# Kernel tuning notes

Measured on AMD Instinct MI355X. Metric: run time of the kernel, lower is better.

Reference implementation:

```python
import jax, jax.numpy as jnp
import numpy as np

N = 100000   # nodes
E = 1600000  # random edges per augmented graph (before self-loops)
F = 128      # input_dim
H = 128      # hidden_dim
K = 3        # n_clusters
L = 3        # num_layers


def setup_inputs() -> dict:
    key = jax.random.key(0)
    ks = jax.random.split(key, 24)
    x1 = jax.random.normal(ks[0], (N, F), jnp.float32)
    x2 = jax.random.normal(ks[1], (N, F), jnp.float32)
    x3 = jax.random.normal(ks[2], (N, F), jnp.float32)
    loops = jnp.arange(N, dtype=jnp.int32)
    self_loops = jnp.stack([loops, loops])  # [2, N]

    def aug_edges(k):
        e = jax.random.randint(k, (2, E), 0, N, dtype=jnp.int32)
        return jnp.concatenate([e, self_loops], axis=1)  # [2, E+N]

    e1 = aug_edges(ks[3])
    e2 = aug_edges(ks[4])
    e3 = aug_edges(ks[5])

    s = 1.0 / np.sqrt(H)
    Ws = jax.random.normal(ks[6], (L, H, H), jnp.float32) * s  # F == H
    bs = jnp.zeros((L, H), jnp.float32)
    a = jnp.float32(0.25)  # PReLU slope (torch default)
    cw1 = jax.random.normal(ks[7], (H, H), jnp.float32) * s
    cb1 = jnp.zeros((H,), jnp.float32)
    cw2 = jax.random.normal(ks[8], (H, K), jnp.float32) * s
    cb2 = jnp.zeros((K,), jnp.float32)
    iw1 = jax.random.normal(ks[9], (H, H), jnp.float32) * s
    ib1 = jnp.zeros((H,), jnp.float32)
    iw2 = jax.random.normal(ks[10], (H, H), jnp.float32) * s
    ib2 = jnp.zeros((H,), jnp.float32)
    return dict(x1=x1, x2=x2, x3=x3, e1=e1, e2=e2, e3=e3,
                Ws=Ws, bs=bs, a=a, cw1=cw1, cb1=cb1, cw2=cw2, cb2=cb2,
                iw1=iw1, ib1=ib1, iw2=iw2, ib2=ib2)


def _l2norm(z):
    # F.normalize(z, dim=1), eps=1e-12
    return z / jnp.maximum(jnp.linalg.norm(z, axis=1, keepdims=True), 1e-12)


def _gconv(x, edges, Ws, bs, a):
    # DGL GraphConv norm='left': messages from src scaled by 1/out_deg(src),
    # summed at dst, then linear + shared PReLU per layer; final row L2-norm.
    src, dst = edges[0], edges[1]
    deg = jax.ops.segment_sum(jnp.ones(src.shape[0], x.dtype), src, num_segments=N)
    inv = 1.0 / jnp.maximum(deg, 1.0)  # DGL clamps zero out-degree
    z = x
    for l in range(L):
        msg = (z * inv[:, None])[src]               # [E, H] gather
        agg = jax.ops.segment_sum(msg, dst, num_segments=N)  # [N, H] scatter-add
        z = agg @ Ws[l] + bs[l]
        z = jnp.where(z >= 0, z, a * z)             # PReLU
    return _l2norm(z)


def reference(x1, x2, x3, e1, e2, e3, Ws, bs, a,
              cw1, cb1, cw2, cb2, iw1, ib1, iw2, ib2):
    z1 = _gconv(x1, e1, Ws, bs, a)
    z2 = _gconv(x2, e2, Ws, bs, a)
    z3 = _gconv(x3, e3, Ws, bs, a)

    def cluster(z):
        h = jax.nn.elu(z @ cw1 + cb1)
        p = jax.nn.softmax(h @ cw2 + cb2, axis=1)
        return _l2norm(p)

    def inst(z):
        return jax.nn.elu(z @ iw1 + ib1) @ iw2 + ib2

    return (z3, inst(z1), inst(z2), cluster(z1), cluster(z2))
```

## Files before the change

### kernel.cpp

```cpp
#include <hip/hip_runtime.h>
#include <hip/hip_bf16.h>
#include <cmath>


typedef __attribute__((ext_vector_type(8))) short short8;
typedef __attribute__((ext_vector_type(4))) float floatx4;

#define NB_MAX 512
#define PART_B 256
#define LCSR_MAX 6144

static __device__ __forceinline__ unsigned short f2bf(float f) {
  unsigned u = __builtin_bit_cast(unsigned, f);
  u += 0x7fffu + ((u >> 16) & 1u);
  return (unsigned short)(u >> 16);
}
static __device__ __forceinline__ float bf2f(unsigned short h) {
  unsigned u = ((unsigned)h) << 16;
  return __builtin_bit_cast(float, u);
}
static __device__ __forceinline__ float bflo(unsigned v) {
  return __builtin_bit_cast(float, v << 16);
}
static __device__ __forceinline__ float bfhi(unsigned v) {
  return __builtin_bit_cast(float, v & 0xffff0000u);
}

static __device__ __forceinline__ floatx4 mfma16(short8 a, short8 b, floatx4 c) {
  return __builtin_amdgcn_mfma_f32_16x16x32_bf16(a, b, c, 0, 0, 0);
}


__global__ __launch_bounds__(256) void bucket_count(const int* __restrict__ src,
                                                    const int* __restrict__ dst,
                                                    int ne, int nb, int chunk,
                                                    int* __restrict__ bcnt,
                                                    int* __restrict__ deg) {
  __shared__ int h[NB_MAX];
  const int t = threadIdx.x, b = blockIdx.x;
  for (int i = t; i < nb; i += 256) h[i] = 0;
  __syncthreads();
  const int start = b * chunk, endi = min(start + chunk, ne);
  for (int i = start + t; i < endi; i += 256) {
    atomicAdd(&h[dst[i] >> 8], 1);
    atomicAdd(&deg[src[i]], 1);
  }
  __syncthreads();
  for (int i = t; i < nb; i += 256) bcnt[i * PART_B + b] = h[i];
}

__global__ __launch_bounds__(256) void partition_edges(
    const int* __restrict__ src, const int* __restrict__ dst, int ne, int nb,
    int chunk, const int* __restrict__ boff, int* __restrict__ part) {
  __shared__ int h[NB_MAX];
  const int t = threadIdx.x, b = blockIdx.x;
  for (int i = t; i < nb; i += 256) h[i] = boff[i * PART_B + b];
  __syncthreads();
  const int start = b * chunk, endi = min(start + chunk, ne);
  for (int i = start + t; i < endi; i += 256) {
    int d = dst[i];
    int gpos = atomicAdd(&h[d >> 8], 1);
    part[gpos] = (src[i] << 8) | (d & 255);
  }
}

__global__ __launch_bounds__(256) void fine_csr(const int* __restrict__ part,
                                                const int* __restrict__ boff,
                                                int nb, int n, int ne,
                                                int* __restrict__ row_ptr,
                                                int* __restrict__ csr) {
  __shared__ int s[256];
  __shared__ int cur[256];
  __shared__ int lcsr[LCSR_MAX];
  const int t = threadIdx.x, b2 = blockIdx.x;
  const int base = boff[b2 * PART_B];
  const int endb = boff[(b2 + 1) * PART_B];
  const int cnt_local = endb - base;
  const int node_base = b2 << 8;

  s[t] = 0;
  __syncthreads();
  for (int i = base + t; i < endb; i += 256) atomicAdd(&s[part[i] & 255], 1);
  __syncthreads();
  for (int d = 1; d < 256; d <<= 1) {
    int v = s[t];
    int a = (t >= d) ? s[t - d] : 0;
    __syncthreads();
    s[t] = v + a;
    __syncthreads();
  }
  int excl = (t == 0) ? 0 : s[t - 1];
  int node = node_base + t;
  if (node <= n) row_ptr[node] = base + excl;
  if (b2 == nb - 1 && t == 0) row_ptr[n] = ne;
  cur[t] = excl;
  __syncthreads();

  if (cnt_local <= LCSR_MAX) {
    for (int i = base + t; i < endb; i += 256) {
      int v = part[i];
      int p = atomicAdd(&cur[v & 255], 1);
      lcsr[p] = v >> 8;
    }
    __syncthreads();
    for (int i = t; i < cnt_local; i += 256) csr[base + i] = lcsr[i];
  } else {
    for (int i = base + t; i < endb; i += 256) {
      int v = part[i];
      int p = atomicAdd(&cur[v & 255], 1);
      csr[base + p] = v >> 8;
    }
  }
}

__global__ __launch_bounds__(256) void make_inv(const int* __restrict__ deg,
                                                float* __restrict__ inv, int n) {
  int i = blockIdx.x * blockDim.x + threadIdx.x;
  if (i < n) inv[i] = 1.0f / (float)(deg[i] + 1);
}

#define SCAN_B 256
#define SCAN_T 256

__global__ __launch_bounds__(SCAN_T) void scan_part(const int* __restrict__ cnt,
                                                    int n, int cpt,
                                                    int* __restrict__ partials) {
  __shared__ int red[SCAN_T];
  const int t = threadIdx.x, b = blockIdx.x;
  const int g = b * SCAN_T + t;
  const int start = g * cpt, endi = min(start + cpt, n);
  int s = 0;
  for (int i = start; i < endi; ++i) s += cnt[i];
  red[t] = s;
  __syncthreads();
  for (int d = SCAN_T / 2; d > 0; d >>= 1) {
    if (t < d) red[t] += red[t + d];
    __syncthreads();
  }
  if (t == 0) partials[b] = red[0];
}

__global__ __launch_bounds__(SCAN_B) void scan_offsets(
    const int* __restrict__ partials, int* __restrict__ block_off,
    int* __restrict__ row_ptr, int n) {
  __shared__ int sums[SCAN_B];
  const int t = threadIdx.x;
  sums[t] = partials[t];
  __syncthreads();
  for (int d = 1; d < SCAN_B; d <<= 1) {
    int v = sums[t];
    int a = (t >= d) ? sums[t - d] : 0;
    __syncthreads();
    sums[t] = v + a;
    __syncthreads();
  }
  block_off[t] = (t == 0) ? 0 : sums[t - 1];
  if (t == SCAN_B - 1) row_ptr[n] = sums[t];
}

__global__ __launch_bounds__(SCAN_T) void scan_fill(const int* __restrict__ cnt,
                                                    int n, int cpt,
                                                    const int* __restrict__ block_off,
                                                    int* __restrict__ row_ptr) {
  __shared__ int sums[SCAN_T];
  const int t = threadIdx.x, b = blockIdx.x;
  const int g = b * SCAN_T + t;
  const int start = g * cpt, endi = min(start + cpt, n);
  int s = 0;
  for (int i = start; i < endi; ++i) s += cnt[i];
  sums[t] = s;
  __syncthreads();
  for (int d = 1; d < SCAN_T; d <<= 1) {
    int v = sums[t];
    int a = (t >= d) ? sums[t - d] : 0;
    __syncthreads();
    sums[t] = v + a;
    __syncthreads();
  }
  int off = block_off[b] + ((t == 0) ? 0 : sums[t - 1]);
  for (int i = start; i < endi; ++i) {
    row_ptr[i] = off;
    off += cnt[i];
  }
}


__global__ __launch_bounds__(256) void scale_cast(const float* __restrict__ x,
                                                  const float* __restrict__ inv,
                                                  unsigned short* __restrict__ zsc,
                                                  int n) {
  int idx = blockIdx.x * blockDim.x + threadIdx.x;
  if (idx >= n * 32) return;
  int row = idx >> 5;
  float s = inv[row];
  float4 v = *(const float4*)(x + (size_t)idx * 4);
  unsigned u0 = (unsigned)f2bf(v.x * s) | ((unsigned)f2bf(v.y * s) << 16);
  unsigned u1 = (unsigned)f2bf(v.z * s) | ((unsigned)f2bf(v.w * s) << 16);
  uint2 p = {u0, u1};
  *(uint2*)(zsc + (size_t)idx * 4) = p;
}

__global__ __launch_bounds__(256) void prep_w(const float* __restrict__ src,
                                              unsigned short* __restrict__ dh,
                                              unsigned short* __restrict__ dl) {
  int idx = blockIdx.x * 256 + threadIdx.x;
  int k = idx >> 7, nn = idx & 127;
  float w = src[idx];
  unsigned short h = f2bf(w);
  dh[nn * 128 + k] = h;
  dl[nn * 128 + k] = f2bf(w - bf2f(h));
}


__global__ __launch_bounds__(256) void aggregate_bf16(
    const unsigned short* __restrict__ zsc, const int* __restrict__ row_ptr,
    const int* __restrict__ csr_src, unsigned short* __restrict__ ah, int n) {
  int w = (blockIdx.x * blockDim.x + threadIdx.x) >> 6;
  const int lane = threadIdx.x & 63;
  if (w >= n) return;
  w = __builtin_amdgcn_readfirstlane(w);
  const int beg = row_ptr[w], end = row_ptr[w + 1];
  const unsigned* zp = (const unsigned*)zsc;
  unsigned vs = zp[(size_t)w * 64 + lane];
  float ax0 = bflo(vs), ay0 = bfhi(vs), ax1 = 0.f, ay1 = 0.f;
  float ax2 = 0.f, ay2 = 0.f, ax3 = 0.f, ay3 = 0.f;
  for (int base = beg; base < end; base += 64) {
    const int cnt = min(64, end - base);
    int my = (base + lane < end) ? csr_src[base + lane] : 0;
    int e = 0;
    for (; e + 8 <= cnt; e += 8) {
      int s0 = __shfl(my, e);
      int s1 = __shfl(my, e + 1);
      int s2 = __shfl(my, e + 2);
      int s3 = __shfl(my, e + 3);
      int s4 = __shfl(my, e + 4);
      int s5 = __shfl(my, e + 5);
      int s6 = __shfl(my, e + 6);
      int s7 = __shfl(my, e + 7);
      unsigned v0 = zp[(size_t)s0 * 64 + lane];
      unsigned v1 = zp[(size_t)s1 * 64 + lane];
      unsigned v2 = zp[(size_t)s2 * 64 + lane];
      unsigned v3 = zp[(size_t)s3 * 64 + lane];
      unsigned v4 = zp[(size_t)s4 * 64 + lane];
      unsigned v5 = zp[(size_t)s5 * 64 + lane];
      unsigned v6 = zp[(size_t)s6 * 64 + lane];
      unsigned v7 = zp[(size_t)s7 * 64 + lane];
      ax0 += bflo(v0); ay0 += bfhi(v0);
      ax1 += bflo(v1); ay1 += bfhi(v1);
      ax2 += bflo(v2); ay2 += bfhi(v2);
      ax3 += bflo(v3); ay3 += bfhi(v3);
      ax0 += bflo(v4); ay0 += bfhi(v4);
      ax1 += bflo(v5); ay1 += bfhi(v5);
      ax2 += bflo(v6); ay2 += bfhi(v6);
      ax3 += bflo(v7); ay3 += bfhi(v7);
    }
    for (; e + 4 <= cnt; e += 4) {
      int s0 = __shfl(my, e);
      int s1 = __shfl(my, e + 1);
      int s2 = __shfl(my, e + 2);
      int s3 = __shfl(my, e + 3);
      unsigned v0 = zp[(size_t)s0 * 64 + lane];
      unsigned v1 = zp[(size_t)s1 * 64 + lane];
      unsigned v2 = zp[(size_t)s2 * 64 + lane];
      unsigned v3 = zp[(size_t)s3 * 64 + lane];
      ax0 += bflo(v0); ay0 += bfhi(v0);
      ax1 += bflo(v1); ay1 += bfhi(v1);
      ax2 += bflo(v2); ay2 += bfhi(v2);
      ax3 += bflo(v3); ay3 += bfhi(v3);
    }
    for (; e < cnt; ++e) {
      int s0 = __shfl(my, e);
      unsigned v0 = zp[(size_t)s0 * 64 + lane];
      ax0 += bflo(v0);
      ay0 += bfhi(v0);
    }
  }
  float ax = (ax0 + ax1) + (ax2 + ax3);
  float ay = (ay0 + ay1) + (ay2 + ay3);
  ((unsigned*)ah)[(size_t)w * 64 + lane] =
      (unsigned)f2bf(ax) | ((unsigned)f2bf(ay) << 16);
}

template <int MODE>
__global__ __launch_bounds__(256) void gemm_one(
    const unsigned short* __restrict__ Ah,
    const unsigned short* __restrict__ Wth, const unsigned short* __restrict__ Wtl,
    const float* __restrict__ bias, float* __restrict__ outf,
    unsigned short* __restrict__ o_h,
    const float* __restrict__ inv, const float* __restrict__ slope_ptr,
    const float* __restrict__ cw2, const float* __restrict__ cb2, int n) {
  const int tid = threadIdx.x;
  const int wave = tid >> 6, lane = tid & 63;
  const int lr = lane & 15;
  const int lg = lane >> 4;
  const int m0 = blockIdx.x * 128 + wave * 32;

  floatx4 acc[2][8];
#pragma unroll
  for (int mf = 0; mf < 2; ++mf)
#pragma unroll
    for (int nf = 0; nf < 8; ++nf) acc[mf][nf] = (floatx4){0.f, 0.f, 0.f, 0.f};

#pragma unroll
  for (int ks = 0; ks < 4; ++ks) {
    short8 a_h[2];
#pragma unroll
    for (int mf = 0; mf < 2; ++mf) {
      size_t aoff = (size_t)(m0 + mf * 16 + lr) * 128 + ks * 32 + lg * 8;
      a_h[mf] = *(const short8*)(Ah + aoff);
    }
#pragma unroll
    for (int nf = 0; nf < 8; ++nf) {
      size_t boff = (size_t)(nf * 16 + lr) * 128 + ks * 32 + lg * 8;
      short8 b_h = *(const short8*)(Wth + boff);
      short8 b_l = *(const short8*)(Wtl + boff);
#pragma unroll
      for (int mf = 0; mf < 2; ++mf) {
        acc[mf][nf] = mfma16(a_h[mf], b_h, acc[mf][nf]);
        acc[mf][nf] = mfma16(a_h[mf], b_l, acc[mf][nf]);
      }
    }
  }

  float bv[8];
#pragma unroll
  for (int nf = 0; nf < 8; ++nf) bv[nf] = bias[nf * 16 + lr];
  float slope = 0.f;
  if constexpr (MODE <= 2) slope = *slope_ptr;
  float c2v[8][3];
  if constexpr (MODE == 5) {
#pragma unroll
    for (int nf = 0; nf < 8; ++nf) {
      int col = nf * 16 + lr;
#pragma unroll
      for (int c = 0; c < 3; ++c) c2v[nf][c] = cw2[col * 3 + c];
    }
  }

#pragma unroll
  for (int mf = 0; mf < 2; ++mf) {
#pragma unroll
    for (int reg = 0; reg < 4; ++reg) {
      const int row = m0 + mf * 16 + lg * 4 + reg;
      float v[8];
#pragma unroll
      for (int nf = 0; nf < 8; ++nf) {
        float t = acc[mf][nf][reg] + bv[nf];
        if constexpr (MODE <= 2) t = (t >= 0.f) ? t : t * slope;
        if constexpr (MODE == 3 || MODE == 5) t = (t > 0.f) ? t : expm1f(t);
        v[nf] = t;
      }
      if constexpr (MODE == 0) {
        float s = inv[row < n ? row : 0];
#pragma unroll
        for (int nf = 0; nf < 8; ++nf)
          o_h[(size_t)row * 128 + nf * 16 + lr] = f2bf(v[nf] * s);
      } else if constexpr (MODE == 1 || MODE == 2) {
        float ss = 0.f;
#pragma unroll
        for (int nf = 0; nf < 8; ++nf) ss = fmaf(v[nf], v[nf], ss);
        ss += __shfl_xor(ss, 1);
        ss += __shfl_xor(ss, 2);
        ss += __shfl_xor(ss, 4);
        ss += __shfl_xor(ss, 8);
        float r = 1.f / fmaxf(sqrtf(ss), 1e-12f);
        if constexpr (MODE == 1) {
          if (row < n) {
#pragma unroll
            for (int nf = 0; nf < 8; ++nf)
              outf[(size_t)row * 128 + nf * 16 + lr] = v[nf] * r;
          }
        } else {
#pragma unroll
          for (int nf = 0; nf < 8; ++nf)
            o_h[(size_t)row * 128 + nf * 16 + lr] = f2bf(v[nf] * r);
        }
      } else if constexpr (MODE == 3) {
#pragma unroll
        for (int nf = 0; nf < 8; ++nf)
          o_h[(size_t)row * 128 + nf * 16 + lr] = f2bf(v[nf]);
      } else if constexpr (MODE == 4) {
        if (row < n) {
#pragma unroll
          for (int nf = 0; nf < 8; ++nf)
            outf[(size_t)row * 128 + nf * 16 + lr] = v[nf];
        }
      } else if constexpr (MODE == 5) {
        float p[3] = {0.f, 0.f, 0.f};
#pragma unroll
        for (int nf = 0; nf < 8; ++nf)
#pragma unroll
          for (int c = 0; c < 3; ++c) p[c] = fmaf(v[nf], c2v[nf][c], p[c]);
#pragma unroll
        for (int c = 0; c < 3; ++c) {
          p[c] += __shfl_xor(p[c], 1);
          p[c] += __shfl_xor(p[c], 2);
          p[c] += __shfl_xor(p[c], 4);
          p[c] += __shfl_xor(p[c], 8);
          p[c] += cb2[c];
        }
        float mx = fmaxf(p[0], fmaxf(p[1], p[2]));
        float e0 = expf(p[0] - mx), e1 = expf(p[1] - mx), e2 = expf(p[2] - mx);
        float sden = e0 + e1 + e2;
        float q0 = e0 / sden, q1 = e1 / sden, q2 = e2 / sden;
        float nr =
            1.f / fmaxf(sqrtf(fmaf(q0, q0, fmaf(q1, q1, q2 * q2))), 1e-12f);
        if (row < n && lr < 3) {
          float val = (lr == 0) ? q0 * nr : (lr == 1) ? q1 * nr : q2 * nr;
          outf[(size_t)row * 3 + lr] = val;
        }
      }
    }
  }
}


extern "C" void kernel_launch(void* const* d_in, const int* in_sizes, int n_in,
                              void* d_out, int out_size, void* d_ws,
                              size_t ws_size, hipStream_t stream) {
  const int H = 128;
  const int N = in_sizes[0] / H;
  const int Npad = (N + 127) & ~127;
  const int NB = (N + 255) >> 8;

  char* ws = (char*)d_ws;
  size_t off = 0;
  auto take = [&](size_t bytes) -> void* {
    void* p = ws + off;
    off = (off + bytes + 255) & ~(size_t)255;
    return p;
  };
  float* inv = (float*)take((size_t)N * 4);
  int* deg = (int*)take((size_t)N * 4);
  int* row_ptr = (int*)take((size_t)(N + 1) * 4);
  int* bcnt = (int*)take((size_t)NB * PART_B * 4);
  int* boff = (int*)take(((size_t)NB * PART_B + 1) * 4);
  int* partials = (int*)take((size_t)SCAN_B * 4);
  int* block_off = (int*)take((size_t)SCAN_B * 4);
  int ne_max = 0;
  for (int g = 0; g < 3; ++g) ne_max = max(ne_max, in_sizes[3 + g] / 2);
  int* csr = (int*)take((size_t)ne_max * 4);
  int* part = (int*)take((size_t)ne_max * 4);
  unsigned short* wth = (unsigned short*)take((size_t)6 * 16384 * 2);
  unsigned short* wtl = (unsigned short*)take((size_t)6 * 16384 * 2);
  unsigned short* ah = (unsigned short*)take((size_t)Npad * 128 * 2);
  unsigned short* zsc = (unsigned short*)take((size_t)Npad * 128 * 2);

  const float* Ws = (const float*)d_in[6];
  const float* bs = (const float*)d_in[7];
  const float* a_ptr = (const float*)d_in[8];
  const float* cw1 = (const float*)d_in[9];
  const float* cb1 = (const float*)d_in[10];
  const float* cw2 = (const float*)d_in[11];
  const float* cb2 = (const float*)d_in[12];
  const float* iw1 = (const float*)d_in[13];
  const float* ib1 = (const float*)d_in[14];
  const float* iw2 = (const float*)d_in[15];
  const float* ib2 = (const float*)d_in[16];

  float* outp = (float*)d_out;
  float* out_z3 = outp;
  float* out_inst[2] = {outp + (size_t)N * H, outp + 2 * (size_t)N * H};
  float* out_clu[2] = {outp + 3 * (size_t)N * H,
                       outp + 3 * (size_t)N * H + (size_t)N * 3};

  const float* wsrc[6] = {Ws, Ws + 16384, Ws + 2 * 16384, iw1, iw2, cw1};
  for (int m = 0; m < 6; ++m)
    prep_w<<<64, 256, 0, stream>>>(wsrc[m], wth + m * 16384, wtl + m * 16384);

  const int aggBlocks = (N + 3) / 4;
  const int gemmBlocks = Npad / 128;
  const int nscan = NB * PART_B;
  const int cpt = (nscan + SCAN_B * SCAN_T - 1) / (SCAN_B * SCAN_T);

  for (int g = 0; g < 3; ++g) {
    const float* x = (const float*)d_in[g];
    const int* edges = (const int*)d_in[3 + g];
    const int ne = in_sizes[3 + g] / 2;
    const int neR = (ne > N) ? (ne - N) : 0;
    const int* src = edges;
    const int* dst = edges + ne;
    const int chunk = (neR + PART_B - 1) / PART_B;

    hipMemsetAsync(deg, 0, (size_t)N * 4, stream);
    bucket_count<<<PART_B, 256, 0, stream>>>(src, dst, neR, NB, chunk, bcnt,
                                             deg);
    make_inv<<<(N + 255) / 256, 256, 0, stream>>>(deg, inv, N);
    scan_part<<<SCAN_B, SCAN_T, 0, stream>>>(bcnt, nscan, cpt, partials);
    scan_offsets<<<1, SCAN_B, 0, stream>>>(partials, block_off, boff, nscan);
    scan_fill<<<SCAN_B, SCAN_T, 0, stream>>>(bcnt, nscan, cpt, block_off, boff);
    partition_edges<<<PART_B, 256, 0, stream>>>(src, dst, neR, NB, chunk, boff,
                                                part);
    fine_csr<<<NB, 256, 0, stream>>>(part, boff, NB, N, neR, row_ptr, csr);

    scale_cast<<<(N * 32 + 255) / 256, 256, 0, stream>>>(x, inv, zsc, N);

    for (int l = 0; l < 2; ++l) {
      aggregate_bf16<<<aggBlocks, 256, 0, stream>>>(zsc, row_ptr, csr, ah, N);
      gemm_one<0><<<gemmBlocks, 256, 0, stream>>>(
          ah, wth + l * 16384, wtl + l * 16384, bs + l * 128, nullptr, zsc, inv,
          a_ptr, nullptr, nullptr, N);
    }
    aggregate_bf16<<<aggBlocks, 256, 0, stream>>>(zsc, row_ptr, csr, ah, N);
    if (g == 2) {
      gemm_one<1><<<gemmBlocks, 256, 0, stream>>>(
          ah, wth + 2 * 16384, wtl + 2 * 16384, bs + 2 * 128, out_z3, nullptr,
          nullptr, a_ptr, nullptr, nullptr, N);
    } else {
      gemm_one<2><<<gemmBlocks, 256, 0, stream>>>(
          ah, wth + 2 * 16384, wtl + 2 * 16384, bs + 2 * 128, nullptr, zsc,
          nullptr, a_ptr, nullptr, nullptr, N);
      gemm_one<3><<<gemmBlocks, 256, 0, stream>>>(
          zsc, wth + 3 * 16384, wtl + 3 * 16384, ib1, nullptr, ah, nullptr,
          nullptr, nullptr, nullptr, N);
      gemm_one<4><<<gemmBlocks, 256, 0, stream>>>(
          ah, wth + 4 * 16384, wtl + 4 * 16384, ib2, out_inst[g], nullptr,
          nullptr, nullptr, nullptr, nullptr, N);
      gemm_one<5><<<gemmBlocks, 256, 0, stream>>>(
          zsc, wth + 5 * 16384, wtl + 5 * 16384, cb1, out_clu[g], nullptr,
          nullptr, nullptr, cw2, cb2, N);
    }
  }
}
```

Baseline: 1.569 ms.

## Stage GEMM weights in LDS, deepen aggregate unroll, use fast exp

The GEMM kernel now copies the hi/lo bf16 weight matrices into padded shared memory once per block and reads the B fragments from LDS instead of global memory. The aggregation loop gains a 16-wide batch of gathers to keep more loads in flight, and ELU/softmax switch to __expf. The costs are about 68KB of LDS per block, which limits occupancy, extra register pressure in the aggregate kernel, and slightly lower exp accuracy.

```diff
diff --git a/kernel.cpp b/kernel.cpp
--- a/kernel.cpp
+++ b/kernel.cpp
@@ -9,6 +9,7 @@
 #define NB_MAX 512
 #define PART_B 256
 #define LCSR_MAX 6144
+#define WPAD 136
 
 static __device__ __forceinline__ unsigned short f2bf(float f) {
   unsigned u = __builtin_bit_cast(unsigned, f);
@@ -25,9 +26,39 @@
 static __device__ __forceinline__ float bfhi(unsigned v) {
   return __builtin_bit_cast(float, v & 0xffff0000u);
 }
+static __device__ __forceinline__ float fast_elu(float t) {
+  return (t > 0.f) ? t : (__expf(t) - 1.f);
+}
 
 static __device__ __forceinline__ floatx4 mfma16(short8 a, short8 b, floatx4 c) {
   return __builtin_amdgcn_mfma_f32_16x16x32_bf16(a, b, c, 0, 0, 0);
+}
+
+static __device__ __forceinline__ void stage_w(
+    const unsigned short* __restrict__ g, unsigned short (*l)[WPAD], int tid) {
+#pragma unroll
+  for (int i = 0; i < 8; ++i) {
+    int chunk = tid + (i << 8);
+    int r = chunk >> 4;
+    int c = (chunk & 15) << 3;
+    *(short8*)(&l[r][c]) = *(const short8*)(g + r * 128 + c);
+  }
+}
+
+static __device__ __forceinline__ void mfma_block_l(
+    const short8 a_h[2], const unsigned short (*Wh)[WPAD],
+    const unsigned short (*Wl)[WPAD], int ks, int lr, int lg,
+    floatx4 acc[2][8]) {
+#pragma unroll
+  for (int nf = 0; nf < 8; ++nf) {
+    short8 b_h = *(const short8*)(&Wh[nf * 16 + lr][ks * 32 + lg * 8]);
+    short8 b_l = *(const short8*)(&Wl[nf * 16 + lr][ks * 32 + lg * 8]);
+#pragma unroll
+    for (int mf = 0; mf < 2; ++mf) {
+      acc[mf][nf] = mfma16(a_h[mf], b_h, acc[mf][nf]);
+      acc[mf][nf] = mfma16(a_h[mf], b_l, acc[mf][nf]);
+    }
+  }
 }
 
 
@@ -228,6 +259,21 @@
     const int cnt = min(64, end - base);
     int my = (base + lane < end) ? csr_src[base + lane] : 0;
     int e = 0;
+    for (; e + 16 <= cnt; e += 16) {
+      int s[16];
+      unsigned v[16];
+#pragma unroll
+      for (int i = 0; i < 16; ++i) s[i] = __shfl(my, e + i);
+#pragma unroll
+      for (int i = 0; i < 16; ++i) v[i] = zp[(size_t)s[i] * 64 + lane];
+#pragma unroll
+      for (int i = 0; i < 16; i += 4) {
+        ax0 += bflo(v[i]);     ay0 += bfhi(v[i]);
+        ax1 += bflo(v[i + 1]); ay1 += bfhi(v[i + 1]);
+        ax2 += bflo(v[i + 2]); ay2 += bfhi(v[i + 2]);
+        ax3 += bflo(v[i + 3]); ay3 += bfhi(v[i + 3]);
+      }
+    }
     for (; e + 8 <= cnt; e += 8) {
       int s0 = __shfl(my, e);
       int s1 = __shfl(my, e + 1);
@@ -286,15 +332,21 @@
     const unsigned short* __restrict__ Ah,
     const unsigned short* __restrict__ Wth, const unsigned short* __restrict__ Wtl,
     const float* __restrict__ bias, float* __restrict__ outf,
-    unsigned short* __restrict__ o_h,
-    const float* __restrict__ inv, const float* __restrict__ slope_ptr,
-    const float* __restrict__ cw2, const float* __restrict__ cb2, int n) {
+    unsigned short* __restrict__ o_h, const float* __restrict__ inv,
+    const float* __restrict__ slope_ptr, const float* __restrict__ cw2,
+    const float* __restrict__ cb2, int n) {
+  __shared__ unsigned short lwh[128][WPAD];
+  __shared__ unsigned short lwl[128][WPAD];
   const int tid = threadIdx.x;
   const int wave = tid >> 6, lane = tid & 63;
   const int lr = lane & 15;
   const int lg = lane >> 4;
   const int m0 = blockIdx.x * 128 + wave * 32;
 
+  stage_w(Wth, lwh, tid);
+  stage_w(Wtl, lwl, tid);
+  __syncthreads();
+
   floatx4 acc[2][8];
 #pragma unroll
   for (int mf = 0; mf < 2; ++mf)
@@ -309,17 +361,7 @@
       size_t aoff = (size_t)(m0 + mf * 16 + lr) * 128 + ks * 32 + lg * 8;
       a_h[mf] = *(const short8*)(Ah + aoff);
     }
-#pragma unroll
-    for (int nf = 0; nf < 8; ++nf) {
-      size_t boff = (size_t)(nf * 16 + lr) * 128 + ks * 32 + lg * 8;
-      short8 b_h = *(const short8*)(Wth + boff);
-      short8 b_l = *(const short8*)(Wtl + boff);
-#pragma unroll
-      for (int mf = 0; mf < 2; ++mf) {
-        acc[mf][nf] = mfma16(a_h[mf], b_h, acc[mf][nf]);
-        acc[mf][nf] = mfma16(a_h[mf], b_l, acc[mf][nf]);
-      }
-    }
+    mfma_block_l(a_h, lwh, lwl, ks, lr, lg, acc);
   }
 
   float bv[8];
@@ -347,7 +389,7 @@
       for (int nf = 0; nf < 8; ++nf) {
         float t = acc[mf][nf][reg] + bv[nf];
         if constexpr (MODE <= 2) t = (t >= 0.f) ? t : t * slope;
-        if constexpr (MODE == 3 || MODE == 5) t = (t > 0.f) ? t : expm1f(t);
+        if constexpr (MODE == 3 || MODE == 5) t = fast_elu(t);
         v[nf] = t;
       }
       if constexpr (MODE == 0) {
@@ -400,7 +442,8 @@
           p[c] += cb2[c];
         }
         float mx = fmaxf(p[0], fmaxf(p[1], p[2]));
-        float e0 = expf(p[0] - mx), e1 = expf(p[1] - mx), e2 = expf(p[2] - mx);
+        float e0 = __expf(p[0] - mx), e1 = __expf(p[1] - mx),
+              e2 = __expf(p[2] - mx);
         float sden = e0 + e1 + e2;
         float q0 = e0 / sden, q1 = e1 / sden, q2 = e2 / sden;
         float nr =
```

After: 1.258 ms. 19.8% less time.
